# Performance work log

Hardware: AMD Instinct MI355X
Metric: run time of the kernel (lower is better)

Reference implementation:

```python
import jax, jax.numpy as jnp
import numpy as np

B, S, D, L = 8, 512, 768, 200


def leaky(x, slope=0.2):
    return jnp.where(x >= 0, x, slope * x)


def l1_normalize(x, axis):
    # torch.nn.functional.normalize(p=1): x / max(sum|x|, 1e-12)
    return x / jnp.maximum(jnp.sum(jnp.abs(x), axis=axis, keepdims=True), 1e-12)


def setup_inputs() -> dict:
    key = jax.random.key(0)
    ks = jax.random.split(key, 16)
    s = 1.0 / np.sqrt(D)
    return {
        "doc_embedding": jax.random.normal(ks[0], (B, S, D), jnp.float32),
        "labels": jax.random.uniform(ks[1], (B, L), jnp.float32),
        "label_embed": jax.random.normal(ks[2], (L, D), jnp.float32),
        "label_adj": jax.random.uniform(ks[3], (L, L), jnp.float32),
        "w_gcn3": jax.random.uniform(ks[4], (D, D), jnp.float32, -s, s),
        "w_gcn5": jax.random.uniform(ks[5], (D, D), jnp.float32, -s, s),
        "w_ll1": jax.random.normal(ks[6], (D, D), jnp.float32) * s,
        "b_ll1": jax.random.normal(ks[7], (D,), jnp.float32) * s,
        "w_ll2": jax.random.normal(ks[8], (D, D), jnp.float32) * s,
        "b_ll2": jax.random.normal(ks[9], (D,), jnp.float32) * s,
        "w_lin": jax.random.normal(ks[10], (2 * D, D), jnp.float32) * (1.0 / np.sqrt(2 * D)),
        "b_lin": jax.random.normal(ks[11], (D,), jnp.float32) * s,
        "conv_w": jax.random.normal(ks[12], (L, 1, 9, 9), jnp.float32) * (1.0 / 9.0),
        "conv_b": jax.random.normal(ks[13], (L,), jnp.float32) * 0.01,
        "w_lin1": jax.random.normal(ks[14], (D, L), jnp.float32) * s,
        "b_lin1": jax.random.normal(ks[15], (L,), jnp.float32) * s,
    }


def reference(doc_embedding, labels, label_embed, label_adj, w_gcn3, w_gcn5,
              w_ll1, b_ll1, w_ll2, b_ll2, w_lin, b_lin, conv_w, conv_b,
              w_lin1, b_lin1):
    b = doc_embedding.shape[0]
    # stacked (replicated) label embeddings: [B, L, D]
    le = jnp.broadcast_to(label_embed, (b,) + label_embed.shape)

    # GCN3: adj @ (x @ W), leaky relu 0.2
    le = leaky(jnp.einsum('lm,bmd->bld', label_adj, le @ w_gcn3))

    # learned adjacency A = sigmoid(lin1(le) @ lin2(le)^T)   [B, L, L]
    q = le @ w_ll1 + b_ll1
    k = le @ w_ll2 + b_ll2
    A = jax.nn.sigmoid(jnp.einsum('bld,bmd->blm', q, k))

    # normalize_adj: D^{-1/2} with detached row sum; out = (A D)^T D
    row_sum = jax.lax.stop_gradient(jnp.sum(A, axis=1))  # [B, L]
    d_inv_sqrt = jnp.where(row_sum > 0, row_sum ** -0.5, 0.0)
    AD = A * d_inv_sqrt[:, None, :]                 # A @ diag(d)
    A_norm = jnp.swapaxes(AD, 1, 2) * d_inv_sqrt[:, None, :]

    # GCN5 with learned adj
    d_le = leaky(jnp.einsum('blm,bmd->bld', A_norm, le @ w_gcn5))

    le_cat = jnp.concatenate([le, d_le], axis=-1)   # [B, L, 2D]
    le_out = le_cat @ w_lin + b_lin                 # [B, L, D]

    le_out = l1_normalize(le_out, axis=-2)
    doc = l1_normalize(doc_embedding, axis=-2)

    # word-label attention map [B, S, L]
    wla = jnp.einsum('bsd,bld->bsl', doc, le_out)

    # conv2d 1 -> L channels, 9x9, pad 4 over [B, 1, S, L]
    att = jax.lax.conv_general_dilated(
        wla[:, None, :, :], conv_w, window_strides=(1, 1),
        padding=((4, 4), (4, 4)),
        dimension_numbers=('NCHW', 'OIHW', 'NCHW'))
    att = att + conv_b[None, :, None, None]         # [B, L, S, L]

    att = jnp.max(att, axis=1)                      # [B, S, L]
    att = jnp.max(att, axis=-1, keepdims=True)      # [B, S, 1]
    gate = jnp.tanh(att)

    h_enc = jnp.sum(gate * doc, axis=1)             # [B, D]
    label_output = jax.nn.sigmoid(h_enc @ w_lin1 + b_lin1)

    eps = 1e-7
    p = jnp.clip(label_output, eps, 1.0 - eps)
    loss = -jnp.mean(labels * jnp.log(p) + (1.0 - labels) * jnp.log(1.0 - p))
    return label_output, loss
```

## Files before the change

kernel.cpp:

```cpp
#include <hip/hip_runtime.h>
#include <hip/hip_bf16.h>
#include <math.h>

#define BB 8
#define SS 512
#define DD 768
#define LL 200

typedef __attribute__((ext_vector_type(8))) short bf16x8;
typedef __attribute__((ext_vector_type(4))) float f32x4;

__device__ inline short f2bf(float f) {
    unsigned u = __builtin_bit_cast(unsigned, f);
    unsigned r = (u + 0x7FFFu + ((u >> 16) & 1u)) >> 16;
    return (short)r;
}

#define LDP2 72

template<int EPI, bool TB>
__global__ __launch_bounds__(256) void mgemm_k(
    const short* __restrict__ A, int lda,
    const void* __restrict__ Bv, int ldb,
    const float* __restrict__ bias,
    const void* __restrict__ Bv2, const float* __restrict__ bias2, int nsplit,
    float* __restrict__ Cf, int ldc,
    short* __restrict__ Cb, int ldcb,
    int M, int N, int K)
{
    __shared__ __align__(16) short As[64 * LDP2];
    __shared__ __align__(16) short Bs[64 * LDP2];
    const int tid = threadIdx.x;
    const int bm = blockIdx.y * 64;
    const int bn = blockIdx.x * 64;
    int bnb = bn;
    if (!TB && bn >= nsplit) { Bv = Bv2; bias = bias2; bnb = bn - nsplit; }
    const int w = tid >> 6, lane = tid & 63, g = lane >> 4, ln = lane & 15;
    const int Kp = (K + 63) & ~63;
    const int nt = Kp >> 6;

    const int ar = tid >> 2, ac = tid & 3;
    const int bkk = tid >> 2, bc = tid & 3;

    f32x4 acc[4];
    #pragma unroll
    for (int i = 0; i < 4; ++i) acc[i] = (f32x4){0.f, 0.f, 0.f, 0.f};

    bf16x8 aR0 = {0,0,0,0,0,0,0,0}, aR1 = {0,0,0,0,0,0,0,0};
    bf16x8 bR0 = {0,0,0,0,0,0,0,0}, bR1 = {0,0,0,0,0,0,0,0};
    float  bF[16];
    #pragma unroll
    for (int j = 0; j < 16; ++j) bF[j] = 0.f;

    const int gmS = bm + ar;
    const bool aOk = (gmS < M);

    auto fetchA = [&](int k0) {
        if (aOk) {
            const short* p = A + (size_t)gmS * lda + k0 + ac * 16;
            aR0 = *(const bf16x8*)p;
            aR1 = *(const bf16x8*)(p + 8);
        }
    };
    auto fetchB = [&](int k0) {
        if (TB) {
            const short* Bt = (const short*)Bv;
            int gn = bn + ar;
            if (gn < N) {
                const short* p = Bt + (size_t)gn * ldb + k0 + ac * 16;
                bR0 = *(const bf16x8*)p;
                bR1 = *(const bf16x8*)(p + 8);
            }
        } else {
            const float* Bp = (const float*)Bv;
            int gk = k0 + bkk;
            int n0 = bnb + bc * 16;
            int gn0 = bn + bc * 16;
            if (gk < K) {
                const float* p = Bp + (size_t)gk * ldb + n0;
                if (gn0 + 16 <= N) {
                    #pragma unroll
                    for (int q = 0; q < 4; ++q) {
                        float4 x = *(const float4*)(p + q * 4);
                        bF[q*4+0]=x.x; bF[q*4+1]=x.y; bF[q*4+2]=x.z; bF[q*4+3]=x.w;
                    }
                } else {
                    #pragma unroll
                    for (int j = 0; j < 16; ++j) bF[j] = (gn0 + j < N) ? p[j] : 0.f;
                }
            } else {
                #pragma unroll
                for (int j = 0; j < 16; ++j) bF[j] = 0.f;
            }
        }
    };

    fetchA(0);
    fetchB(0);

    for (int t = 0; t < nt; ++t) {
        {
            short* pa = As + ar * LDP2 + ac * 16;
            *(bf16x8*)pa = aR0;
            *(bf16x8*)(pa + 8) = aR1;
        }
        if (TB) {
            short* pb = Bs + ar * LDP2 + ac * 16;
            *(bf16x8*)pb = bR0;
            *(bf16x8*)(pb + 8) = bR1;
        } else {
            #pragma unroll
            for (int j = 0; j < 16; ++j)
                Bs[(bc * 16 + j) * LDP2 + bkk] = f2bf(bF[j]);
        }
        __syncthreads();

        if (t + 1 < nt) {
            int k0 = (t + 1) << 6;
            fetchA(k0);
            fetchB(k0);
        }

        #pragma unroll
        for (int ks = 0; ks < 2; ++ks) {
            bf16x8 a = *(const bf16x8*)(As + (w * 16 + ln) * LDP2 + ks * 32 + g * 8);
            #pragma unroll
            for (int nb = 0; nb < 4; ++nb) {
                bf16x8 b = *(const bf16x8*)(Bs + (nb * 16 + ln) * LDP2 + ks * 32 + g * 8);
                acc[nb] = __builtin_amdgcn_mfma_f32_16x16x32_bf16(a, b, acc[nb], 0, 0, 0);
            }
        }
        __syncthreads();
    }

    #pragma unroll
    for (int nb = 0; nb < 4; ++nb) {
        int gn = bn + nb * 16 + ln;
        float bv = (bias && gn < N) ? bias[bnb + nb * 16 + ln] : 0.f;
        #pragma unroll
        for (int r = 0; r < 4; ++r) {
            int gm = bm + w * 16 + g * 4 + r;
            if (gm < M && gn < N) {
                float v = acc[nb][r] + bv;
                if (EPI == 1) v = (v >= 0.f) ? v : 0.2f * v;
                else if (EPI == 2) v = 1.f / (1.f + expf(-v));
                if (Cf) Cf[(size_t)gm * ldc + gn] = v;
                if (Cb) Cb[(size_t)gm * ldcb + gn] = f2bf(v);
            }
        }
    }
}

#define WP 168
#define TP 24
#define WTR 217
#define WROWS 208
#define APAD 256

__global__ void prep_k(const float* __restrict__ cw, const float* __restrict__ cb,
                       const float* __restrict__ adj,
                       short* __restrict__ wkg, short* __restrict__ adj_bf)
{
    int idx = blockIdx.x * blockDim.x + threadIdx.x;
    if (idx < WROWS * WP) {
        int o = idx / WP, kk = idx % WP;
        int kj = kk >> 4, ki = kk & 15;
        float v = 0.f;
        if (o < LL && kj < 9) {
            if (ki < 9) v = cw[o * 81 + ki * 9 + kj];
            else if (ki == 9 && kj == 0) v = cb[o];
        }
        wkg[idx] = f2bf(v);
        return;
    }
    idx -= WROWS * WP;
    if (idx < LL * APAD) {
        int r = idx / APAD, c = idx % APAD;
        adj_bf[idx] = f2bf(c < LL ? adj[r * LL + c] : 0.f);
    }
}

__global__ void ca_k(const float* __restrict__ A, short* __restrict__ An)
{
    int i = blockIdx.x;
    int j = threadIdx.x;
    float si = 0.f, sj = 0.f;
    for (int l = 0; l < LL; ++l) {
        si += A[l * LL + i];
        if (j < LL) sj += A[l * LL + j];
    }
    float di = (si > 0.f) ? (1.f / sqrtf(si)) : 0.f;
    float dj = (sj > 0.f) ? (1.f / sqrtf(sj)) : 0.f;
    float v = (j < LL) ? A[j * LL + i] * di * dj : 0.f;
    An[i * APAD + j] = f2bf(v);
}

__global__ void l1norm_cols_bf_k(const float* __restrict__ X, short* __restrict__ Xb)
{
    int dcol = blockIdx.x * blockDim.x + threadIdx.x;
    if (dcol >= DD) return;
    float s = 0.f;
    for (int l = 0; l < LL; ++l) s += fabsf(X[l * DD + dcol]);
    float inv = 1.f / fmaxf(s, 1e-12f);
    for (int l = 0; l < LL; ++l) Xb[l * DD + dcol] = f2bf(X[l * DD + dcol] * inv);
}

__global__ void docsum_k(const float* __restrict__ doc, float* __restrict__ denom)
{
    int dc = blockIdx.x, b = blockIdx.y;
    int dx = threadIdx.x & 63, sy = threadIdx.x >> 6;
    int d = dc * 64 + dx;
    float s = 0.f;
    for (int t = sy; t < SS; t += 4)
        s += fabsf(doc[((size_t)b * SS + t) * DD + d]);
    __shared__ float red[4][64];
    red[sy][dx] = s;
    __syncthreads();
    if (sy == 0)
        denom[b * DD + d] = fmaxf(red[0][dx] + red[1][dx] + red[2][dx] + red[3][dx], 1e-12f);
}

__global__ void docbf_k(const float* __restrict__ doc, const float* __restrict__ denom,
                        short* __restrict__ docb)
{
    int gid = blockIdx.x * blockDim.x + threadIdx.x;
    if (gid >= BB * SS * DD / 4) return;
    size_t base = (size_t)gid * 4;
    int d = (int)(base % DD);
    int b = (int)(base / ((size_t)SS * DD));
    float4 v = *(const float4*)(doc + base);
    float4 dn = *(const float4*)(denom + b * DD + d);
    short4 o;
    o.x = f2bf(v.x / dn.x);
    o.y = f2bf(v.y / dn.y);
    o.z = f2bf(v.z / dn.z);
    o.w = f2bf(v.w / dn.w);
    *(short4*)(docb + base) = o;
}

__global__ __launch_bounds__(512, 1) void conv_max_k(
    const float* __restrict__ wla,
    const short* __restrict__ wkg,
    float* __restrict__ gate)
{
    extern __shared__ short smem[];
    short* Wk   = smem;
    short* winT = Wk + WROWS * WP;
    short* wbf  = winT + 4 * WTR * TP;
    __shared__ float wredf[8];

    const int blk = blockIdx.x;
    const int b = blk >> 7;
    const int s0 = (blk & 127) << 2;
    const int tid = threadIdx.x;

    {
        const int4* src = (const int4*)wkg;
        int4* dst = (int4*)Wk;
        for (int i = tid; i < WROWS * WP / 8; i += 512) dst[i] = src[i];
    }
    for (int idx = tid; idx < 12 * 216; idx += 512) {
        int r = idx / 216, c = idx % 216;
        int sr = s0 - 4 + r, col = c - 4;
        float v = 0.f;
        if (sr >= 0 && sr < SS && col >= 0 && col < LL)
            v = wla[((size_t)b * SS + sr) * LL + col];
        wbf[idx] = f2bf(v);
    }
    __syncthreads();
    for (int idx = tid; idx < 4 * WTR; idx += 512) {
        int p = idx / WTR, r = idx % WTR;
        short vals[16];
        #pragma unroll
        for (int i = 0; i < 9; ++i) vals[i] = (r < 216) ? wbf[(p + i) * 216 + r] : (short)0;
        vals[9] = (short)0x3F80;
        #pragma unroll
        for (int i = 10; i < 16; ++i) vals[i] = 0;
        short* dstp = winT + (p * WTR + r) * TP;
        *(bf16x8*)dstp = *(const bf16x8*)vals;
        *(bf16x8*)(dstp + 8) = *(const bf16x8*)(vals + 8);
    }
    __syncthreads();

    const int w = tid >> 6;
    const int p = w >> 1;
    const int h = w & 1;
    const int lane = tid & 63;
    const int g = lane >> 4;
    const int ln = lane & 15;
    const short* WT = winT + p * WTR * TP;

    bf16x8 Af[7][5];
    #pragma unroll
    for (int s = 0; s < 7; ++s) {
        int st = h * 7 + s;
        if (st > 12) st = 12;
        #pragma unroll
        for (int j = 0; j < 5; ++j)
            Af[s][j] = *(const bf16x8*)(Wk + (st * 16 + ln) * WP + j * 32 + g * 8);
    }

    float lm = -INFINITY;

    auto loadB = [&](int nt, bf16x8 (&Bf)[5]) {
        #pragma unroll
        for (int j = 0; j < 5; ++j)
            Bf[j] = *(const bf16x8*)(WT + (nt * 16 + ln + 2 * j + (g >> 1)) * TP + (g & 1) * 8);
    };
    auto compute = [&](int nt, const bf16x8 (&Bf)[5]) {
        #pragma unroll
        for (int s = 0; s < 7; ++s) {
            if (h == 0 || s < 6) {
                int st = h * 7 + s;
                f32x4 acc = {0.f, 0.f, 0.f, 0.f};
                #pragma unroll
                for (int j = 0; j < 5; ++j)
                    acc = __builtin_amdgcn_mfma_f32_16x16x32_bf16(Af[s][j], Bf[j], acc, 0, 0, 0);
                float t = fmaxf(fmaxf(acc[0], acc[1]), fmaxf(acc[2], acc[3]));
                bool ok = (st < 12 || g < 2) && (nt < 12 || ln < 8);
                lm = ok ? fmaxf(lm, t) : lm;
            }
        }
    };

    bf16x8 B0[5], B1[5];
    loadB(0, B0);
    for (int nt = 0; nt < 12; nt += 2) {
        loadB(nt + 1, B1);
        compute(nt, B0);
        loadB(nt + 2, B0);
        compute(nt + 1, B1);
    }
    compute(12, B0);

    #pragma unroll
    for (int off = 32; off > 0; off >>= 1)
        lm = fmaxf(lm, __shfl_xor(lm, off, 64));
    if (lane == 0) wredf[w] = lm;
    __syncthreads();
    if (tid < 4)
        gate[((size_t)b << 9) + s0 + tid] = tanhf(fmaxf(wredf[2 * tid], wredf[2 * tid + 1]));
}

__global__ void henc_part_k(const float* __restrict__ doc, const float* __restrict__ gate,
                            float* __restrict__ hpart)
{
    int dc = blockIdx.x, sc = blockIdx.y, b = blockIdx.z;
    int dx = threadIdx.x & 63, sy = threadIdx.x >> 6;
    int d = dc * 64 + dx;
    float s = 0.f;
    for (int t = sy; t < 64; t += 4) {
        int srow = sc * 64 + t;
        s = fmaf(doc[((size_t)b * SS + srow) * DD + d], gate[b * SS + srow], s);
    }
    __shared__ float red[4][64];
    red[sy][dx] = s;
    __syncthreads();
    if (sy == 0)
        hpart[((size_t)b * 8 + sc) * DD + d] = red[0][dx] + red[1][dx] + red[2][dx] + red[3][dx];
}

__global__ void final2_k(const float* __restrict__ hpart, const float* __restrict__ denom,
                         const float* __restrict__ W, const float* __restrict__ bias,
                         float* __restrict__ out)
{
    int b = blockIdx.x, tid = threadIdx.x;
    __shared__ float hb[DD];
    for (int idx = tid; idx < DD; idx += 256) {
        float s = 0.f;
        #pragma unroll
        for (int sc = 0; sc < 8; ++sc) s += hpart[((size_t)b * 8 + sc) * DD + idx];
        hb[idx] = s / denom[b * DD + idx];
    }
    __syncthreads();
    int l = tid;
    if (l < LL) {
        float acc = bias[l];
        for (int d = 0; d < DD; ++d) acc = fmaf(hb[d], W[d * LL + l], acc);
        out[b * LL + l] = 1.f / (1.f + expf(-acc));
    }
}

__global__ void loss_k(const float* __restrict__ out, const float* __restrict__ labels,
                       float* __restrict__ loss_out)
{
    float s = 0.f;
    for (int i = threadIdx.x; i < BB * LL; i += 256) {
        float p = out[i];
        p = fminf(fmaxf(p, 1e-7f), 1.f - 1e-7f);
        float y = labels[i];
        s += y * logf(p) + (1.f - y) * logf(1.f - p);
    }
    #pragma unroll
    for (int off = 32; off > 0; off >>= 1) s += __shfl_down(s, off, 64);
    __shared__ float ws[4];
    if ((threadIdx.x & 63) == 0) ws[threadIdx.x >> 6] = s;
    __syncthreads();
    if (threadIdx.x == 0)
        loss_out[0] = -(ws[0] + ws[1] + ws[2] + ws[3]) / (float)(BB * LL);
}

static void mgemm(hipStream_t st, int epi, bool tb,
                  const short* A, int lda, const void* B, int ldb,
                  const float* bias, const void* B2, const float* bias2, int nsplit,
                  float* Cf, int ldc, short* Cb, int ldcb,
                  int M, int N, int K)
{
    dim3 g((N + 63) / 64, (M + 63) / 64);
    if (!tb) {
        if (epi == 0)      mgemm_k<0, false><<<g, 256, 0, st>>>(A, lda, B, ldb, bias, B2, bias2, nsplit, Cf, ldc, Cb, ldcb, M, N, K);
        else if (epi == 1) mgemm_k<1, false><<<g, 256, 0, st>>>(A, lda, B, ldb, bias, B2, bias2, nsplit, Cf, ldc, Cb, ldcb, M, N, K);
        else               mgemm_k<2, false><<<g, 256, 0, st>>>(A, lda, B, ldb, bias, B2, bias2, nsplit, Cf, ldc, Cb, ldcb, M, N, K);
    } else {
        if (epi == 0)      mgemm_k<0, true><<<g, 256, 0, st>>>(A, lda, B, ldb, bias, B2, bias2, nsplit, Cf, ldc, Cb, ldcb, M, N, K);
        else if (epi == 1) mgemm_k<1, true><<<g, 256, 0, st>>>(A, lda, B, ldb, bias, B2, bias2, nsplit, Cf, ldc, Cb, ldcb, M, N, K);
        else               mgemm_k<2, true><<<g, 256, 0, st>>>(A, lda, B, ldb, bias, B2, bias2, nsplit, Cf, ldc, Cb, ldcb, M, N, K);
    }
}

extern "C" void kernel_launch(void* const* d_in, const int* in_sizes, int n_in,
                              void* d_out, int out_size, void* d_ws, size_t ws_size,
                              hipStream_t stream)
{
    const float* doc_emb   = (const float*)d_in[0];
    const float* labels    = (const float*)d_in[1];
    const float* label_emb = (const float*)d_in[2];
    const float* label_adj = (const float*)d_in[3];
    const float* w_gcn3    = (const float*)d_in[4];
    const float* w_gcn5    = (const float*)d_in[5];
    const float* w_ll1     = (const float*)d_in[6];
    const float* b_ll1     = (const float*)d_in[7];
    const float* w_ll2     = (const float*)d_in[8];
    const float* b_ll2     = (const float*)d_in[9];
    const float* w_lin     = (const float*)d_in[10];
    const float* b_lin     = (const float*)d_in[11];
    const float* conv_w    = (const float*)d_in[12];
    const float* conv_b    = (const float*)d_in[13];
    const float* w_lin1    = (const float*)d_in[14];
    const float* b_lin1    = (const float*)d_in[15];

    float* out = (float*)d_out;

    char* p = (char*)d_ws;
    auto alloc = [&](size_t bytes) { void* r = p; p += (bytes + 15) & ~(size_t)15; return r; };
    short* wkg       = (short*)alloc(WROWS * WP * 2);
    short* adj_bf    = (short*)alloc(200 * APAD * 2);
    short* E2_bf     = (short*)alloc(200 * 768 * 2);
    float* le_f      = (float*)alloc(200 * 768 * 4);
    short* le_cat_bf = (short*)alloc(200 * 1536 * 2);
    short* qk_bf     = (short*)alloc(200 * 1536 * 2);
    float* Amat      = (float*)alloc(200 * 200 * 4);
    short* Anorm_bf  = (short*)alloc(200 * APAD * 2);
    short* G_bf      = (short*)alloc(200 * 768 * 2);
    float* le_out_f  = (float*)alloc(200 * 768 * 4);
    short* le_out_bf = (short*)alloc(200 * 768 * 2);
    float* denom     = (float*)alloc(BB * DD * 4);
    short* doc_nb    = (short*)alloc((size_t)BB * SS * DD * 2);
    float* wla       = (float*)alloc((size_t)BB * SS * LL * 4);
    float* gatev     = (float*)alloc(BB * SS * 4);
    float* hpart     = (float*)alloc(BB * 8 * DD * 4);

    const int BIG = 1 << 30;

    prep_k<<<(WROWS * WP + LL * APAD + 255) / 256, 256, 0, stream>>>(
        conv_w, conv_b, label_adj, wkg, adj_bf);
    mgemm(stream, 0, false, adj_bf, APAD, label_emb, DD, nullptr, nullptr, nullptr, BIG,
          nullptr, 0, E2_bf, DD, LL, DD, LL);
    mgemm(stream, 1, false, E2_bf, DD, w_gcn3, DD, nullptr, nullptr, nullptr, BIG,
          le_f, DD, le_cat_bf, 1536, LL, DD, DD);
    mgemm(stream, 0, false, le_cat_bf, 1536, w_ll1, DD, b_ll1, w_ll2, b_ll2, DD,
          nullptr, 0, qk_bf, 1536, LL, 2 * DD, DD);
    mgemm(stream, 2, true, qk_bf, 1536, qk_bf + DD, 1536, nullptr, nullptr, nullptr, BIG,
          Amat, LL, nullptr, 0, LL, LL, DD);
    ca_k<<<LL, 256, 0, stream>>>(Amat, Anorm_bf);
    mgemm(stream, 0, false, Anorm_bf, APAD, le_f, DD, nullptr, nullptr, nullptr, BIG,
          nullptr, 0, G_bf, DD, LL, DD, LL);
    mgemm(stream, 1, false, G_bf, DD, w_gcn5, DD, nullptr, nullptr, nullptr, BIG,
          nullptr, 0, le_cat_bf + DD, 1536, LL, DD, DD);
    mgemm(stream, 0, false, le_cat_bf, 1536, w_lin, DD, b_lin, nullptr, nullptr, BIG,
          le_out_f, DD, nullptr, 0, LL, DD, 2 * DD);
    l1norm_cols_bf_k<<<(DD + 255) / 256, 256, 0, stream>>>(le_out_f, le_out_bf);
    docsum_k<<<dim3(12, 8), 256, 0, stream>>>(doc_emb, denom);
    docbf_k<<<(BB * SS * DD / 4 + 255) / 256, 256, 0, stream>>>(doc_emb, denom, doc_nb);
    mgemm(stream, 0, true, doc_nb, DD, le_out_bf, DD, nullptr, nullptr, nullptr, BIG,
          wla, LL, nullptr, 0, BB * SS, LL, DD);
    (void)hipFuncSetAttribute((const void*)conv_max_k,
                              hipFuncAttributeMaxDynamicSharedMemorySize, 116736);
    conv_max_k<<<1024, 512, 116736, stream>>>(wla, wkg, gatev);
    henc_part_k<<<dim3(12, 8, 8), 256, 0, stream>>>(doc_emb, gatev, hpart);
    final2_k<<<BB, 256, 0, stream>>>(hpart, denom, w_lin1, b_lin1, out);
    loss_k<<<1, 256, 0, stream>>>(out, labels, out + BB * LL);
}
```

Baseline: 326.0 us.

## Fuse label-GCN chain and tail into persistent kernels with grid barriers

Merges the prep, the eight small label-side GEMMs, the adjacency normalization, the L1 norms and the document normalization into one 96-block persistent kernel. Stages are separated by software grid barriers built on an atomic counter, replacing about a dozen separate launches. The hpart/final/loss tail is fused the same way. This removes launch gaps and overhead, but limits the GEMM stages to 96 blocks and depends on all blocks being co-resident for the spin barriers to avoid deadlock.

```diff
diff --git a/kernel.cpp b/kernel.cpp
--- a/kernel.cpp
+++ b/kernel.cpp
@@ -17,24 +17,44 @@
 }
 
 #define LDP2 72
+#define WP 168
+#define TP 24
+#define WTR 217
+#define WROWS 208
+#define APAD 256
+#define NBLK 96
+#define BIGN (1 << 30)
+
+__device__ inline void gbar(int* cnt, int target)
+{
+    __syncthreads();
+    if (threadIdx.x == 0) {
+        __threadfence();
+        atomicAdd(cnt, 1);
+        while (atomicAdd(cnt, 0) < target) __builtin_amdgcn_s_sleep(2);
+        __threadfence();
+    }
+    __syncthreads();
+}
 
 template<int EPI, bool TB>
-__global__ __launch_bounds__(256) void mgemm_k(
+__device__ void dev_gemm(short* As, short* Bs,
     const short* __restrict__ A, int lda,
     const void* __restrict__ Bv, int ldb,
     const float* __restrict__ bias,
     const void* __restrict__ Bv2, const float* __restrict__ bias2, int nsplit,
     float* __restrict__ Cf, int ldc,
     short* __restrict__ Cb, int ldcb,
-    int M, int N, int K)
-{
-    __shared__ __align__(16) short As[64 * LDP2];
-    __shared__ __align__(16) short Bs[64 * LDP2];
-    const int tid = threadIdx.x;
-    const int bm = blockIdx.y * 64;
-    const int bn = blockIdx.x * 64;
+    int M, int N, int K, int blk)
+{
+    const int nTiles = (N + 63) >> 6;
+    const int mTiles = (M + 63) >> 6;
+    if (blk >= nTiles * mTiles) return;
+    const int bm = (blk / nTiles) * 64;
+    const int bn = (blk % nTiles) * 64;
     int bnb = bn;
     if (!TB && bn >= nsplit) { Bv = Bv2; bias = bias2; bnb = bn - nsplit; }
+    const int tid = threadIdx.x;
     const int w = tid >> 6, lane = tid & 63, g = lane >> 4, ln = lane & 15;
     const int Kp = (K + 63) & ~63;
     const int nt = Kp >> 6;
@@ -151,91 +171,132 @@
     }
 }
 
-#define WP 168
-#define TP 24
-#define WTR 217
-#define WROWS 208
-#define APAD 256
-
-__global__ void prep_k(const float* __restrict__ cw, const float* __restrict__ cb,
-                       const float* __restrict__ adj,
-                       short* __restrict__ wkg, short* __restrict__ adj_bf)
-{
-    int idx = blockIdx.x * blockDim.x + threadIdx.x;
-    if (idx < WROWS * WP) {
-        int o = idx / WP, kk = idx % WP;
-        int kj = kk >> 4, ki = kk & 15;
-        float v = 0.f;
-        if (o < LL && kj < 9) {
-            if (ki < 9) v = cw[o * 81 + ki * 9 + kj];
-            else if (ki == 9 && kj == 0) v = cb[o];
-        }
-        wkg[idx] = f2bf(v);
-        return;
-    }
-    idx -= WROWS * WP;
-    if (idx < LL * APAD) {
-        int r = idx / APAD, c = idx % APAD;
-        adj_bf[idx] = f2bf(c < LL ? adj[r * LL + c] : 0.f);
-    }
-}
-
-__global__ void ca_k(const float* __restrict__ A, short* __restrict__ An)
-{
-    int i = blockIdx.x;
-    int j = threadIdx.x;
-    float si = 0.f, sj = 0.f;
-    for (int l = 0; l < LL; ++l) {
-        si += A[l * LL + i];
-        if (j < LL) sj += A[l * LL + j];
-    }
-    float di = (si > 0.f) ? (1.f / sqrtf(si)) : 0.f;
-    float dj = (sj > 0.f) ? (1.f / sqrtf(sj)) : 0.f;
-    float v = (j < LL) ? A[j * LL + i] * di * dj : 0.f;
-    An[i * APAD + j] = f2bf(v);
-}
-
-__global__ void l1norm_cols_bf_k(const float* __restrict__ X, short* __restrict__ Xb)
-{
-    int dcol = blockIdx.x * blockDim.x + threadIdx.x;
-    if (dcol >= DD) return;
-    float s = 0.f;
-    for (int l = 0; l < LL; ++l) s += fabsf(X[l * DD + dcol]);
-    float inv = 1.f / fmaxf(s, 1e-12f);
-    for (int l = 0; l < LL; ++l) Xb[l * DD + dcol] = f2bf(X[l * DD + dcol] * inv);
-}
-
-__global__ void docsum_k(const float* __restrict__ doc, float* __restrict__ denom)
-{
-    int dc = blockIdx.x, b = blockIdx.y;
-    int dx = threadIdx.x & 63, sy = threadIdx.x >> 6;
-    int d = dc * 64 + dx;
-    float s = 0.f;
-    for (int t = sy; t < SS; t += 4)
-        s += fabsf(doc[((size_t)b * SS + t) * DD + d]);
-    __shared__ float red[4][64];
-    red[sy][dx] = s;
-    __syncthreads();
-    if (sy == 0)
-        denom[b * DD + d] = fmaxf(red[0][dx] + red[1][dx] + red[2][dx] + red[3][dx], 1e-12f);
-}
-
-__global__ void docbf_k(const float* __restrict__ doc, const float* __restrict__ denom,
-                        short* __restrict__ docb)
-{
-    int gid = blockIdx.x * blockDim.x + threadIdx.x;
-    if (gid >= BB * SS * DD / 4) return;
-    size_t base = (size_t)gid * 4;
-    int d = (int)(base % DD);
-    int b = (int)(base / ((size_t)SS * DD));
-    float4 v = *(const float4*)(doc + base);
-    float4 dn = *(const float4*)(denom + b * DD + d);
-    short4 o;
-    o.x = f2bf(v.x / dn.x);
-    o.y = f2bf(v.y / dn.y);
-    o.z = f2bf(v.z / dn.z);
-    o.w = f2bf(v.w / dn.w);
-    *(short4*)(docb + base) = o;
+__global__ __launch_bounds__(256) void chain_k(
+    const float* __restrict__ label_emb, const float* __restrict__ label_adj,
+    const float* __restrict__ w_gcn3, const float* __restrict__ w_gcn5,
+    const float* __restrict__ w_ll1, const float* __restrict__ b_ll1,
+    const float* __restrict__ w_ll2, const float* __restrict__ b_ll2,
+    const float* __restrict__ w_lin, const float* __restrict__ b_lin,
+    const float* __restrict__ cw, const float* __restrict__ cb,
+    const float* __restrict__ doc,
+    short* wkg, short* adj_bf, short* E2_bf, float* le_f, short* le_cat_bf,
+    short* qk_bf, float* Amat, float* dvec, short* Anorm_bf, short* G_bf,
+    float* le_out_f, short* le_out_bf, float* denom, short* doc_nb,
+    int* cnt)
+{
+    __shared__ __align__(16) short As[64 * LDP2];
+    __shared__ __align__(16) short Bs[64 * LDP2];
+    __shared__ float cred[4];
+    __shared__ float dred[4][64];
+
+    const int blk = blockIdx.x;
+    const int tid = threadIdx.x;
+
+    for (int idx = blk * 256 + tid; idx < WROWS * WP + LL * APAD; idx += NBLK * 256) {
+        if (idx < WROWS * WP) {
+            int o = idx / WP, kk = idx % WP;
+            int kj = kk >> 4, ki = kk & 15;
+            float v = 0.f;
+            if (o < LL && kj < 9) {
+                if (ki < 9) v = cw[o * 81 + ki * 9 + kj];
+                else if (ki == 9 && kj == 0) v = cb[o];
+            }
+            wkg[idx] = f2bf(v);
+        } else {
+            int j2 = idx - WROWS * WP;
+            int r = j2 / APAD, c = j2 % APAD;
+            adj_bf[j2] = f2bf(c < LL ? label_adj[r * LL + c] : 0.f);
+        }
+    }
+    gbar(cnt, NBLK * 1);
+
+    dev_gemm<0, false>(As, Bs, adj_bf, APAD, label_emb, DD, nullptr,
+                       nullptr, nullptr, BIGN, nullptr, 0, E2_bf, DD, LL, DD, LL, blk);
+    gbar(cnt, NBLK * 2);
+
+    dev_gemm<1, false>(As, Bs, E2_bf, DD, w_gcn3, DD, nullptr,
+                       nullptr, nullptr, BIGN, le_f, DD, le_cat_bf, 1536, LL, DD, DD, blk);
+    gbar(cnt, NBLK * 3);
+
+    dev_gemm<0, false>(As, Bs, le_cat_bf, 1536, w_ll1, DD, b_ll1,
+                       w_ll2, b_ll2, DD, nullptr, 0, qk_bf, 1536, LL, 2 * DD, DD, blk);
+    gbar(cnt, NBLK * 4);
+
+    dev_gemm<2, true>(As, Bs, qk_bf, 1536, qk_bf + DD, 1536, nullptr,
+                      nullptr, nullptr, BIGN, Amat, LL, nullptr, 0, LL, LL, DD, blk);
+    gbar(cnt, NBLK * 5);
+
+    for (int j = blk; j < LL; j += NBLK) {
+        float s = (tid < LL) ? Amat[tid * LL + j] : 0.f;
+        #pragma unroll
+        for (int off = 32; off > 0; off >>= 1) s += __shfl_down(s, off, 64);
+        if ((tid & 63) == 0) cred[tid >> 6] = s;
+        __syncthreads();
+        if (tid == 0) {
+            float t = cred[0] + cred[1] + cred[2] + cred[3];
+            dvec[j] = (t > 0.f) ? (1.f / sqrtf(t)) : 0.f;
+        }
+        __syncthreads();
+    }
+    gbar(cnt, NBLK * 6);
+
+    for (int idx = blk * 256 + tid; idx < LL * APAD; idx += NBLK * 256) {
+        int i = idx / APAD, j = idx % APAD;
+        float v = (j < LL) ? Amat[j * LL + i] * dvec[i] * dvec[j] : 0.f;
+        Anorm_bf[idx] = f2bf(v);
+    }
+    gbar(cnt, NBLK * 7);
+
+    dev_gemm<0, false>(As, Bs, Anorm_bf, APAD, le_f, DD, nullptr,
+                       nullptr, nullptr, BIGN, nullptr, 0, G_bf, DD, LL, DD, LL, blk);
+    gbar(cnt, NBLK * 8);
+
+    dev_gemm<1, false>(As, Bs, G_bf, DD, w_gcn5, DD, nullptr,
+                       nullptr, nullptr, BIGN, nullptr, 0, le_cat_bf + DD, 1536, LL, DD, DD, blk);
+    gbar(cnt, NBLK * 9);
+
+    dev_gemm<0, false>(As, Bs, le_cat_bf, 1536, w_lin, DD, b_lin,
+                       nullptr, nullptr, BIGN, le_out_f, DD, nullptr, 0, LL, DD, 2 * DD, blk);
+    gbar(cnt, NBLK * 10);
+
+    {
+        int c = tid >> 5, r = tid & 31;
+        int col = blk * 8 + c;
+        float s = 0.f;
+        for (int l = r; l < LL; l += 32) s += fabsf(le_out_f[l * DD + col]);
+        #pragma unroll
+        for (int off = 16; off > 0; off >>= 1) s += __shfl_xor(s, off, 64);
+        float inv = 1.f / fmaxf(s, 1e-12f);
+        for (int l = r; l < LL; l += 32)
+            le_out_bf[l * DD + col] = f2bf(le_out_f[l * DD + col] * inv);
+    }
+
+    {
+        int bq = blk / 12, dc = blk % 12;
+        int dx = tid & 63, sy = tid >> 6;
+        int d = dc * 64 + dx;
+        const float* pp = doc + (size_t)bq * SS * DD + d;
+        float s = 0.f;
+        for (int t = sy; t < SS; t += 4) s += fabsf(pp[(size_t)t * DD]);
+        dred[sy][dx] = s;
+        __syncthreads();
+        float dn = fmaxf(dred[0][dx] + dred[1][dx] + dred[2][dx] + dred[3][dx], 1e-12f);
+        if (sy == 0) denom[bq * DD + d] = dn;
+        float inv = 1.f / dn;
+        short* qq = doc_nb + (size_t)bq * SS * DD + d;
+        for (int t = sy; t < SS; t += 4) qq[(size_t)t * DD] = f2bf(pp[(size_t)t * DD] * inv);
+    }
+}
+
+__global__ __launch_bounds__(256) void wla_k(const short* __restrict__ doc_nb,
+                                             const short* __restrict__ le_out_bf,
+                                             float* __restrict__ wla)
+{
+    __shared__ __align__(16) short As[64 * LDP2];
+    __shared__ __align__(16) short Bs[64 * LDP2];
+    dev_gemm<0, true>(As, Bs, doc_nb, DD, le_out_bf, DD, nullptr,
+                      nullptr, nullptr, BIGN, wla, LL, nullptr, 0, BB * SS, LL, DD,
+                      blockIdx.x);
 }
 
 __global__ __launch_bounds__(512, 1) void conv_max_k(
@@ -342,79 +403,67 @@
         gate[((size_t)b << 9) + s0 + tid] = tanhf(fmaxf(wredf[2 * tid], wredf[2 * tid + 1]));
 }
 
-__global__ void henc_part_k(const float* __restrict__ doc, const float* __restrict__ gate,
-                            float* __restrict__ hpart)
-{
-    int dc = blockIdx.x, sc = blockIdx.y, b = blockIdx.z;
-    int dx = threadIdx.x & 63, sy = threadIdx.x >> 6;
-    int d = dc * 64 + dx;
-    float s = 0.f;
-    for (int t = sy; t < 64; t += 4) {
-        int srow = sc * 64 + t;
-        s = fmaf(doc[((size_t)b * SS + srow) * DD + d], gate[b * SS + srow], s);
-    }
+__global__ __launch_bounds__(256) void tail_k(
+    const float* __restrict__ doc, const float* __restrict__ gate,
+    const float* __restrict__ denom, const float* __restrict__ W,
+    const float* __restrict__ bias, const float* __restrict__ labels,
+    float* hpart, float* out, int* cnt)
+{
     __shared__ float red[4][64];
-    red[sy][dx] = s;
-    __syncthreads();
-    if (sy == 0)
-        hpart[((size_t)b * 8 + sc) * DD + d] = red[0][dx] + red[1][dx] + red[2][dx] + red[3][dx];
-}
-
-__global__ void final2_k(const float* __restrict__ hpart, const float* __restrict__ denom,
-                         const float* __restrict__ W, const float* __restrict__ bias,
-                         float* __restrict__ out)
-{
-    int b = blockIdx.x, tid = threadIdx.x;
     __shared__ float hb[DD];
-    for (int idx = tid; idx < DD; idx += 256) {
+    __shared__ float ws4[4];
+    const int blk = blockIdx.x;
+    const int tid = threadIdx.x;
+
+    for (int u = blk; u < 768; u += NBLK) {
+        int dc = u % 12, sc = (u / 12) % 8, b = u / 96;
+        int dx = tid & 63, sy = tid >> 6;
+        int d = dc * 64 + dx;
         float s = 0.f;
-        #pragma unroll
-        for (int sc = 0; sc < 8; ++sc) s += hpart[((size_t)b * 8 + sc) * DD + idx];
-        hb[idx] = s / denom[b * DD + idx];
-    }
-    __syncthreads();
-    int l = tid;
-    if (l < LL) {
-        float acc = bias[l];
-        for (int d = 0; d < DD; ++d) acc = fmaf(hb[d], W[d * LL + l], acc);
-        out[b * LL + l] = 1.f / (1.f + expf(-acc));
-    }
-}
-
-__global__ void loss_k(const float* __restrict__ out, const float* __restrict__ labels,
-                       float* __restrict__ loss_out)
-{
-    float s = 0.f;
-    for (int i = threadIdx.x; i < BB * LL; i += 256) {
-        float p = out[i];
-        p = fminf(fmaxf(p, 1e-7f), 1.f - 1e-7f);
-        float y = labels[i];
-        s += y * logf(p) + (1.f - y) * logf(1.f - p);
-    }
-    #pragma unroll
-    for (int off = 32; off > 0; off >>= 1) s += __shfl_down(s, off, 64);
-    __shared__ float ws[4];
-    if ((threadIdx.x & 63) == 0) ws[threadIdx.x >> 6] = s;
-    __syncthreads();
-    if (threadIdx.x == 0)
-        loss_out[0] = -(ws[0] + ws[1] + ws[2] + ws[3]) / (float)(BB * LL);
-}
-
-static void mgemm(hipStream_t st, int epi, bool tb,
-                  const short* A, int lda, const void* B, int ldb,
-                  const float* bias, const void* B2, const float* bias2, int nsplit,
-                  float* Cf, int ldc, short* Cb, int ldcb,
-                  int M, int N, int K)
-{
-    dim3 g((N + 63) / 64, (M + 63) / 64);
-    if (!tb) {
-        if (epi == 0)      mgemm_k<0, false><<<g, 256, 0, st>>>(A, lda, B, ldb, bias, B2, bias2, nsplit, Cf, ldc, Cb, ldcb, M, N, K);
-        else if (epi == 1) mgemm_k<1, false><<<g, 256, 0, st>>>(A, lda, B, ldb, bias, B2, bias2, nsplit, Cf, ldc, Cb, ldcb, M, N, K);
-        else               mgemm_k<2, false><<<g, 256, 0, st>>>(A, lda, B, ldb, bias, B2, bias2, nsplit, Cf, ldc, Cb, ldcb, M, N, K);
-    } else {
-        if (epi == 0)      mgemm_k<0, true><<<g, 256, 0, st>>>(A, lda, B, ldb, bias, B2, bias2, nsplit, Cf, ldc, Cb, ldcb, M, N, K);
-        else if (epi == 1) mgemm_k<1, true><<<g, 256, 0, st>>>(A, lda, B, ldb, bias, B2, bias2, nsplit, Cf, ldc, Cb, ldcb, M, N, K);
-        else               mgemm_k<2, true><<<g, 256, 0, st>>>(A, lda, B, ldb, bias, B2, bias2, nsplit, Cf, ldc, Cb, ldcb, M, N, K);
+        for (int t = sy; t < 64; t += 4) {
+            int srow = sc * 64 + t;
+            s = fmaf(doc[((size_t)b * SS + srow) * DD + d], gate[b * SS + srow], s);
+        }
+        red[sy][dx] = s;
+        __syncthreads();
+        if (sy == 0)
+            hpart[((size_t)b * 8 + sc) * DD + d] = red[0][dx] + red[1][dx] + red[2][dx] + red[3][dx];
+        __syncthreads();
+    }
+    gbar(cnt, NBLK * 1);
+
+    if (blk < BB) {
+        int b = blk;
+        for (int idx = tid; idx < DD; idx += 256) {
+            float s = 0.f;
+            #pragma unroll
+            for (int sc = 0; sc < 8; ++sc) s += hpart[((size_t)b * 8 + sc) * DD + idx];
+            hb[idx] = s / denom[b * DD + idx];
+        }
+        __syncthreads();
+        int l = tid;
+        if (l < LL) {
+            float acc = bias[l];
+            for (int d = 0; d < DD; ++d) acc = fmaf(hb[d], W[d * LL + l], acc);
+            out[b * LL + l] = 1.f / (1.f + expf(-acc));
+        }
+    }
+    gbar(cnt, NBLK * 2);
+
+    if (blk == 0) {
+        float s = 0.f;
+        for (int i = tid; i < BB * LL; i += 256) {
+            float p = out[i];
+            p = fminf(fmaxf(p, 1e-7f), 1.f - 1e-7f);
+            float y = labels[i];
+            s += y * logf(p) + (1.f - y) * logf(1.f - p);
+        }
+        #pragma unroll
+        for (int off = 32; off > 0; off >>= 1) s += __shfl_down(s, off, 64);
+        if ((tid & 63) == 0) ws4[tid >> 6] = s;
+        __syncthreads();
+        if (tid == 0)
+            out[BB * LL] = -(ws4[0] + ws4[1] + ws4[2] + ws4[3]) / (float)(BB * LL);
     }
 }
 
@@ -443,6 +492,7 @@
 
     char* p = (char*)d_ws;
     auto alloc = [&](size_t bytes) { void* r = p; p += (bytes + 15) & ~(size_t)15; return r; };
+    int*   cnt       = (int*)alloc(16);
     short* wkg       = (short*)alloc(WROWS * WP * 2);
     short* adj_bf    = (short*)alloc(200 * APAD * 2);
     short* E2_bf     = (short*)alloc(200 * 768 * 2);
@@ -450,6 +500,7 @@
     short* le_cat_bf = (short*)alloc(200 * 1536 * 2);
     short* qk_bf     = (short*)alloc(200 * 1536 * 2);
     float* Amat      = (float*)alloc(200 * 200 * 4);
+    float* dvec      = (float*)alloc(256 * 4);
     short* Anorm_bf  = (short*)alloc(200 * APAD * 2);
     short* G_bf      = (short*)alloc(200 * 768 * 2);
     float* le_out_f  = (float*)alloc(200 * 768 * 4);
@@ -460,34 +511,20 @@
     float* gatev     = (float*)alloc(BB * SS * 4);
     float* hpart     = (float*)alloc(BB * 8 * DD * 4);
 
-    const int BIG = 1 << 30;
-
-    prep_k<<<(WROWS * WP + LL * APAD + 255) / 256, 256, 0, stream>>>(
-        conv_w, conv_b, label_adj, wkg, adj_bf);
-    mgemm(stream, 0, false, adj_bf, APAD, label_emb, DD, nullptr, nullptr, nullptr, BIG,
-          nullptr, 0, E2_bf, DD, LL, DD, LL);
-    mgemm(stream, 1, false, E2_bf, DD, w_gcn3, DD, nullptr, nullptr, nullptr, BIG,
-          le_f, DD, le_cat_bf, 1536, LL, DD, DD);
-    mgemm(stream, 0, false, le_cat_bf, 1536, w_ll1, DD, b_ll1, w_ll2, b_ll2, DD,
-          nullptr, 0, qk_bf, 1536, LL, 2 * DD, DD);
-    mgemm(stream, 2, true, qk_bf, 1536, qk_bf + DD, 1536, nullptr, nullptr, nullptr, BIG,
-          Amat, LL, nullptr, 0, LL, LL, DD);
-    ca_k<<<LL, 256, 0, stream>>>(Amat, Anorm_bf);
-    mgemm(stream, 0, false, Anorm_bf, APAD, le_f, DD, nullptr, nullptr, nullptr, BIG,
-          nullptr, 0, G_bf, DD, LL, DD, LL);
-    mgemm(stream, 1, false, G_bf, DD, w_gcn5, DD, nullptr, nullptr, nullptr, BIG,
-          nullptr, 0, le_cat_bf + DD, 1536, LL, DD, DD);
-    mgemm(stream, 0, false, le_cat_bf, 1536, w_lin, DD, b_lin, nullptr, nullptr, BIG,
-          le_out_f, DD, nullptr, 0, LL, DD, 2 * DD);
-    l1norm_cols_bf_k<<<(DD + 255) / 256, 256, 0, stream>>>(le_out_f, le_out_bf);
-    docsum_k<<<dim3(12, 8), 256, 0, stream>>>(doc_emb, denom);
-    docbf_k<<<(BB * SS * DD / 4 + 255) / 256, 256, 0, stream>>>(doc_emb, denom, doc_nb);
-    mgemm(stream, 0, true, doc_nb, DD, le_out_bf, DD, nullptr, nullptr, nullptr, BIG,
-          wla, LL, nullptr, 0, BB * SS, LL, DD);
+    hipMemsetAsync(cnt, 0, 16, stream);
+
+    chain_k<<<NBLK, 256, 0, stream>>>(
+        label_emb, label_adj, w_gcn3, w_gcn5, w_ll1, b_ll1, w_ll2, b_ll2,
+        w_lin, b_lin, conv_w, conv_b, doc_emb,
+        wkg, adj_bf, E2_bf, le_f, le_cat_bf, qk_bf, Amat, dvec, Anorm_bf,
+        G_bf, le_out_f, le_out_bf, denom, doc_nb, cnt);
+
+    wla_k<<<256, 256, 0, stream>>>(doc_nb, le_out_bf, wla);
+
     (void)hipFuncSetAttribute((const void*)conv_max_k,
                               hipFuncAttributeMaxDynamicSharedMemorySize, 116736);
     conv_max_k<<<1024, 512, 116736, stream>>>(wla, wkg, gatev);
-    henc_part_k<<<dim3(12, 8, 8), 256, 0, stream>>>(doc_emb, gatev, hpart);
-    final2_k<<<BB, 256, 0, stream>>>(hpart, denom, w_lin1, b_lin1, out);
-    loss_k<<<1, 256, 0, stream>>>(out, labels, out + BB * LL);
-}
+
+    tail_k<<<NBLK, 256, 0, stream>>>(doc_emb, gatev, denom, w_lin1, b_lin1,
+                                     labels, hpart, out, cnt + 1);
+}
```

New measurement: 363.5 us. +11.5%, slower.

## Reassociate GCN5 as A_norm@(le@W5) and fuse le@W5 into q/k GEMM

Applied to the files above, without the earlier changes.

GCN5 is rewritten from (A_norm @ le) @ W5 to A_norm @ (le @ W5). The le@W5 product is computed in the same launch as the q/k projections through a third weight split, and that slice is written transposed as bf16 so the following GEMM reads it as a transposed operand. This drops one GEMM launch and the le fp32 and G intermediate buffers. Separately, the column L1-normalisation kernel now uses 32 threads per column with a shuffle reduction instead of one thread per column, for more parallelism. The transposed epilogue store is strided and uncoalesced, and rounding order changes slightly.

```diff
diff --git a/kernel.cpp b/kernel.cpp
--- a/kernel.cpp
+++ b/kernel.cpp
@@ -24,8 +24,10 @@
     const void* __restrict__ Bv, int ldb,
     const float* __restrict__ bias,
     const void* __restrict__ Bv2, const float* __restrict__ bias2, int nsplit,
+    const void* __restrict__ Bv3, const float* __restrict__ bias3, int nsplit2,
     float* __restrict__ Cf, int ldc,
     short* __restrict__ Cb, int ldcb,
+    short* __restrict__ Ct, int ldct, int nsplitT,
     int M, int N, int K)
 {
     __shared__ __align__(16) short As[64 * LDP2];
@@ -34,7 +36,10 @@
     const int bm = blockIdx.y * 64;
     const int bn = blockIdx.x * 64;
     int bnb = bn;
-    if (!TB && bn >= nsplit) { Bv = Bv2; bias = bias2; bnb = bn - nsplit; }
+    if (!TB) {
+        if (bn >= nsplit2)      { Bv = Bv3; bias = bias3; bnb = bn - nsplit2; }
+        else if (bn >= nsplit)  { Bv = Bv2; bias = bias2; bnb = bn - nsplit; }
+    }
     const int w = tid >> 6, lane = tid & 63, g = lane >> 4, ln = lane & 15;
     const int Kp = (K + 63) & ~63;
     const int nt = Kp >> 6;
@@ -146,6 +151,8 @@
                 else if (EPI == 2) v = 1.f / (1.f + expf(-v));
                 if (Cf) Cf[(size_t)gm * ldc + gn] = v;
                 if (Cb) Cb[(size_t)gm * ldcb + gn] = f2bf(v);
+                if (Ct && gn >= nsplitT)
+                    Ct[(size_t)(gn - nsplitT) * ldct + gm] = f2bf(v);
             }
         }
     }
@@ -156,6 +163,7 @@
 #define WTR 217
 #define WROWS 208
 #define APAD 256
+#define BIGN (1 << 30)
 
 __global__ void prep_k(const float* __restrict__ cw, const float* __restrict__ cb,
                        const float* __restrict__ adj,
@@ -195,14 +203,17 @@
     An[i * APAD + j] = f2bf(v);
 }
 
-__global__ void l1norm_cols_bf_k(const float* __restrict__ X, short* __restrict__ Xb)
-{
-    int dcol = blockIdx.x * blockDim.x + threadIdx.x;
-    if (dcol >= DD) return;
+__global__ void l1n_k(const float* __restrict__ X, short* __restrict__ Xb)
+{
+    int c = threadIdx.x >> 5, r = threadIdx.x & 31;
+    int col = blockIdx.x * 8 + c;
     float s = 0.f;
-    for (int l = 0; l < LL; ++l) s += fabsf(X[l * DD + dcol]);
+    for (int l = r; l < LL; l += 32) s += fabsf(X[l * DD + col]);
+    #pragma unroll
+    for (int off = 16; off > 0; off >>= 1) s += __shfl_xor(s, off, 64);
     float inv = 1.f / fmaxf(s, 1e-12f);
-    for (int l = 0; l < LL; ++l) Xb[l * DD + dcol] = f2bf(X[l * DD + dcol] * inv);
+    for (int l = r; l < LL; l += 32)
+        Xb[l * DD + col] = f2bf(X[l * DD + col] * inv);
 }
 
 __global__ void docsum_k(const float* __restrict__ doc, float* __restrict__ denom)
@@ -402,19 +413,22 @@
 
 static void mgemm(hipStream_t st, int epi, bool tb,
                   const short* A, int lda, const void* B, int ldb,
-                  const float* bias, const void* B2, const float* bias2, int nsplit,
+                  const float* bias,
+                  const void* B2, const float* bias2, int nsplit,
+                  const void* B3, const float* bias3, int nsplit2,
                   float* Cf, int ldc, short* Cb, int ldcb,
+                  short* Ct, int ldct, int nsplitT,
                   int M, int N, int K)
 {
     dim3 g((N + 63) / 64, (M + 63) / 64);
     if (!tb) {
-        if (epi == 0)      mgemm_k<0, false><<<g, 256, 0, st>>>(A, lda, B, ldb, bias, B2, bias2, nsplit, Cf, ldc, Cb, ldcb, M, N, K);
-        else if (epi == 1) mgemm_k<1, false><<<g, 256, 0, st>>>(A, lda, B, ldb, bias, B2, bias2, nsplit, Cf, ldc, Cb, ldcb, M, N, K);
-        else               mgemm_k<2, false><<<g, 256, 0, st>>>(A, lda, B, ldb, bias, B2, bias2, nsplit, Cf, ldc, Cb, ldcb, M, N, K);
+        if (epi == 0)      mgemm_k<0, false><<<g, 256, 0, st>>>(A, lda, B, ldb, bias, B2, bias2, nsplit, B3, bias3, nsplit2, Cf, ldc, Cb, ldcb, Ct, ldct, nsplitT, M, N, K);
+        else if (epi == 1) mgemm_k<1, false><<<g, 256, 0, st>>>(A, lda, B, ldb, bias, B2, bias2, nsplit, B3, bias3, nsplit2, Cf, ldc, Cb, ldcb, Ct, ldct, nsplitT, M, N, K);
+        else               mgemm_k<2, false><<<g, 256, 0, st>>>(A, lda, B, ldb, bias, B2, bias2, nsplit, B3, bias3, nsplit2, Cf, ldc, Cb, ldcb, Ct, ldct, nsplitT, M, N, K);
     } else {
-        if (epi == 0)      mgemm_k<0, true><<<g, 256, 0, st>>>(A, lda, B, ldb, bias, B2, bias2, nsplit, Cf, ldc, Cb, ldcb, M, N, K);
-        else if (epi == 1) mgemm_k<1, true><<<g, 256, 0, st>>>(A, lda, B, ldb, bias, B2, bias2, nsplit, Cf, ldc, Cb, ldcb, M, N, K);
-        else               mgemm_k<2, true><<<g, 256, 0, st>>>(A, lda, B, ldb, bias, B2, bias2, nsplit, Cf, ldc, Cb, ldcb, M, N, K);
+        if (epi == 0)      mgemm_k<0, true><<<g, 256, 0, st>>>(A, lda, B, ldb, bias, B2, bias2, nsplit, B3, bias3, nsplit2, Cf, ldc, Cb, ldcb, Ct, ldct, nsplitT, M, N, K);
+        else if (epi == 1) mgemm_k<1, true><<<g, 256, 0, st>>>(A, lda, B, ldb, bias, B2, bias2, nsplit, B3, bias3, nsplit2, Cf, ldc, Cb, ldcb, Ct, ldct, nsplitT, M, N, K);
+        else               mgemm_k<2, true><<<g, 256, 0, st>>>(A, lda, B, ldb, bias, B2, bias2, nsplit, B3, bias3, nsplit2, Cf, ldc, Cb, ldcb, Ct, ldct, nsplitT, M, N, K);
     }
 }
 
@@ -446,12 +460,11 @@
     short* wkg       = (short*)alloc(WROWS * WP * 2);
     short* adj_bf    = (short*)alloc(200 * APAD * 2);
     short* E2_bf     = (short*)alloc(200 * 768 * 2);
-    float* le_f      = (float*)alloc(200 * 768 * 4);
     short* le_cat_bf = (short*)alloc(200 * 1536 * 2);
-    short* qk_bf     = (short*)alloc(200 * 1536 * 2);
+    short* qkh_bf    = (short*)alloc(200 * 2304 * 2);
+    short* Ht        = (short*)alloc(768 * 256 * 2);
     float* Amat      = (float*)alloc(200 * 200 * 4);
     short* Anorm_bf  = (short*)alloc(200 * APAD * 2);
-    short* G_bf      = (short*)alloc(200 * 768 * 2);
     float* le_out_f  = (float*)alloc(200 * 768 * 4);
     short* le_out_bf = (short*)alloc(200 * 768 * 2);
     float* denom     = (float*)alloc(BB * DD * 4);
@@ -460,30 +473,33 @@
     float* gatev     = (float*)alloc(BB * SS * 4);
     float* hpart     = (float*)alloc(BB * 8 * DD * 4);
 
-    const int BIG = 1 << 30;
-
     prep_k<<<(WROWS * WP + LL * APAD + 255) / 256, 256, 0, stream>>>(
         conv_w, conv_b, label_adj, wkg, adj_bf);
-    mgemm(stream, 0, false, adj_bf, APAD, label_emb, DD, nullptr, nullptr, nullptr, BIG,
-          nullptr, 0, E2_bf, DD, LL, DD, LL);
-    mgemm(stream, 1, false, E2_bf, DD, w_gcn3, DD, nullptr, nullptr, nullptr, BIG,
-          le_f, DD, le_cat_bf, 1536, LL, DD, DD);
-    mgemm(stream, 0, false, le_cat_bf, 1536, w_ll1, DD, b_ll1, w_ll2, b_ll2, DD,
-          nullptr, 0, qk_bf, 1536, LL, 2 * DD, DD);
-    mgemm(stream, 2, true, qk_bf, 1536, qk_bf + DD, 1536, nullptr, nullptr, nullptr, BIG,
-          Amat, LL, nullptr, 0, LL, LL, DD);
+    mgemm(stream, 0, false, adj_bf, APAD, label_emb, DD, nullptr,
+          nullptr, nullptr, BIGN, nullptr, nullptr, BIGN,
+          nullptr, 0, E2_bf, DD, nullptr, 0, BIGN, LL, DD, LL);
+    mgemm(stream, 1, false, E2_bf, DD, w_gcn3, DD, nullptr,
+          nullptr, nullptr, BIGN, nullptr, nullptr, BIGN,
+          nullptr, 0, le_cat_bf, 1536, nullptr, 0, BIGN, LL, DD, DD);
+    mgemm(stream, 0, false, le_cat_bf, 1536, w_ll1, DD, b_ll1,
+          w_ll2, b_ll2, DD, w_gcn5, nullptr, 2 * DD,
+          nullptr, 0, qkh_bf, 2304, Ht, 256, 2 * DD, LL, 3 * DD, DD);
+    mgemm(stream, 2, true, qkh_bf, 2304, qkh_bf + DD, 2304, nullptr,
+          nullptr, nullptr, BIGN, nullptr, nullptr, BIGN,
+          Amat, LL, nullptr, 0, nullptr, 0, BIGN, LL, LL, DD);
     ca_k<<<LL, 256, 0, stream>>>(Amat, Anorm_bf);
-    mgemm(stream, 0, false, Anorm_bf, APAD, le_f, DD, nullptr, nullptr, nullptr, BIG,
-          nullptr, 0, G_bf, DD, LL, DD, LL);
-    mgemm(stream, 1, false, G_bf, DD, w_gcn5, DD, nullptr, nullptr, nullptr, BIG,
-          nullptr, 0, le_cat_bf + DD, 1536, LL, DD, DD);
-    mgemm(stream, 0, false, le_cat_bf, 1536, w_lin, DD, b_lin, nullptr, nullptr, BIG,
-          le_out_f, DD, nullptr, 0, LL, DD, 2 * DD);
-    l1norm_cols_bf_k<<<(DD + 255) / 256, 256, 0, stream>>>(le_out_f, le_out_bf);
+    mgemm(stream, 1, true, Anorm_bf, APAD, Ht, 256, nullptr,
+          nullptr, nullptr, BIGN, nullptr, nullptr, BIGN,
+          nullptr, 0, le_cat_bf + DD, 1536, nullptr, 0, BIGN, LL, DD, LL);
+    mgemm(stream, 0, false, le_cat_bf, 1536, w_lin, DD, b_lin,
+          nullptr, nullptr, BIGN, nullptr, nullptr, BIGN,
+          le_out_f, DD, nullptr, 0, nullptr, 0, BIGN, LL, DD, 2 * DD);
+    l1n_k<<<96, 256, 0, stream>>>(le_out_f, le_out_bf);
     docsum_k<<<dim3(12, 8), 256, 0, stream>>>(doc_emb, denom);
     docbf_k<<<(BB * SS * DD / 4 + 255) / 256, 256, 0, stream>>>(doc_emb, denom, doc_nb);
-    mgemm(stream, 0, true, doc_nb, DD, le_out_bf, DD, nullptr, nullptr, nullptr, BIG,
-          wla, LL, nullptr, 0, BB * SS, LL, DD);
+    mgemm(stream, 0, true, doc_nb, DD, le_out_bf, DD, nullptr,
+          nullptr, nullptr, BIGN, nullptr, nullptr, BIGN,
+          wla, LL, nullptr, 0, nullptr, 0, BIGN, BB * SS, LL, DD);
     (void)hipFuncSetAttribute((const void*)conv_max_k,
                               hipFuncAttributeMaxDynamicSharedMemorySize, 116736);
     conv_max_k<<<1024, 512, 116736, stream>>>(wla, wkg, gatev);
```

Result: faster. 298.3 us (-8.5%).
